# Performance work log

Hardware: AMD Instinct MI355X
Metric: run time of the kernel (lower is better)

## Reference

```python
import jax, jax.numpy as jnp
import numpy as np

SCALE = 0.08838834764831845  # 1/sqrt(head_dim=128)


def setup_inputs() -> dict:
    key = jax.random.key(0)
    kq, kk, kv = jax.random.split(key, 3)
    S, H, KVH, D = 2048, 32, 8, 128
    q = jax.random.normal(kq, (S, H, D), dtype=jnp.float32)
    k = jax.random.normal(kk, (S, KVH, D), dtype=jnp.float32)
    v = jax.random.normal(kv, (S, KVH, D), dtype=jnp.float32)
    return {"q": q, "k": k, "v": v}


def reference(q, k, v):
    # Prefill path without block tables -> _fallback_attention(q, k, v, scale, causal=True)
    S, H, D = q.shape
    kvh = k.shape[1]
    rep = H // kvh
    # GQA: repeat_interleave KV heads to match query heads
    k = jnp.repeat(k, rep, axis=1)  # [S, H, D]
    v = jnp.repeat(v, rep, axis=1)  # [S, H, D]
    # scores: [H, Sq, Sk]
    scores = jnp.einsum('qhd,khd->hqk', q, k) * SCALE
    # causal mask (seq_len_q == seq_len_k, diagonal=1 triu masked)
    causal = jnp.tril(jnp.ones((S, S), dtype=bool))
    scores = jnp.where(causal[None, :, :], scores, jnp.finfo(scores.dtype).min)
    attn = jax.nn.softmax(scores, axis=-1)
    out = jnp.einsum('hqk,khd->qhd', attn, v)  # [S, H, D]
    return out
```

## Files before the change

kernel.cpp:

```cpp
#include <hip/hip_runtime.h>


#define SEQ   2048
#define NH    32
#define NKVH  8
#define HD    128
#define BQ    128
#define BK    128
#define KSS   136
#define VTSF  72
#define PSS   72
#define SCALE 0.08838834764831845f
#define QS    (0.08838834764831845f * 1.4426950408889634f)

#define TILE_SH 16384
#define KB_ELEMS (SEQ * NKVH * HD)
#define WS_NEED  (2u * KB_ELEMS * 2u)

typedef __attribute__((ext_vector_type(8)))  short short8;
typedef __attribute__((ext_vector_type(16))) float float16;
typedef __attribute__((ext_vector_type(2)))  unsigned int uint2v;

__device__ __forceinline__ unsigned short f2bf(float f) {
    union { float f; unsigned int i; } x; x.f = f;
    unsigned int r = x.i + 0x7fffu + ((x.i >> 16) & 1u);
    return (unsigned short)(r >> 16);
}
__device__ __forceinline__ unsigned int f2bf2(float lo, float hi) {
    return (unsigned int)f2bf(lo) | ((unsigned int)f2bf(hi) << 16);
}
__device__ __forceinline__ unsigned int cvt_pk_bf16(float lo, float hi) {
    unsigned int r;
    asm("v_cvt_pk_bf16_f32 %0, %1, %2" : "=v"(r) : "v"(lo), "v"(hi));
    return r;
}

__device__ __forceinline__ void gload_lds16(const unsigned short* g, unsigned short* l) {
    __builtin_amdgcn_global_load_lds(
        (const __attribute__((address_space(1))) void*)g,
        (__attribute__((address_space(3))) void*)l, 16, 0, 0);
}

#if __has_builtin(__builtin_amdgcn_permlane32_swap)
#define PLSWAP(a, b, xout, yout) do { \
    uint2v r_ = __builtin_amdgcn_permlane32_swap((a), (b), false, false); \
    (xout) = r_.x; (yout) = r_.y; } while (0)
#else
#define PLSWAP(a, b, xout, yout) do { \
    unsigned int a_ = (a), b_ = (b); \
    asm volatile("s_nop 1\n\tv_permlane32_swap_b32 %0, %1" : "+v"(a_), "+v"(b_)); \
    (xout) = a_; (yout) = b_; } while (0)
#endif

#define MAKE_AF(dst, sv, b) do { \
    const unsigned int p0_ = cvt_pk_bf16(sv[(b) + 0], sv[(b) + 1]); \
    const unsigned int p1_ = cvt_pk_bf16(sv[(b) + 2], sv[(b) + 3]); \
    const unsigned int p2_ = cvt_pk_bf16(sv[(b) + 4], sv[(b) + 5]); \
    const unsigned int p3_ = cvt_pk_bf16(sv[(b) + 6], sv[(b) + 7]); \
    unsigned int w0_, w1_, w2_, w3_; \
    PLSWAP(p0_, p2_, w0_, w2_); \
    PLSWAP(p1_, p3_, w1_, w3_); \
    union { short8 v; unsigned int u[4]; } uu_; \
    uu_.u[0] = w0_; uu_.u[1] = w1_; uu_.u[2] = w2_; uu_.u[3] = w3_; \
    (dst) = uu_.v; } while (0)

__global__ __launch_bounds__(256)
void cvt_kv3(const float* __restrict__ k, const float* __restrict__ v,
             unsigned short* __restrict__ kws, unsigned short* __restrict__ vws)
{
    __shared__ unsigned short tl[128 * 144];
    const int t = threadIdx.x;
    if (blockIdx.x < 128) {
        const int bid = blockIdx.x;
        const int kvh = bid >> 4, tile = bid & 15;
        unsigned short* dst = kws + (size_t)bid * TILE_SH;
        #pragma unroll
        for (int r = 0; r < 8; ++r) {
            const int gid = r * 256 + t;
            const int gl = gid >> 7, row = gid & 127;
            const float* src =
                k + ((size_t)(tile * 128 + row) * NKVH + kvh) * HD + gl * 8;
            const float4 a = *(const float4*)(src);
            const float4 b = *(const float4*)(src + 4);
            uint4 o;
            o.x = f2bf2(a.x, a.y); o.y = f2bf2(a.z, a.w);
            o.z = f2bf2(b.x, b.y); o.w = f2bf2(b.z, b.w);
            *(uint4*)(dst + (size_t)gid * 8) = o;
        }
        return;
    }
    const int bid = blockIdx.x - 128;
    const int kvh = bid >> 4, tile = bid & 15;
    const int dp  = (t & 63) * 2;
    const int k0q = t >> 6;
    #pragma unroll
    for (int r = 0; r < 32; ++r) {
        const int key = k0q + r * 4;
        const float2 a =
            *(const float2*)(v + ((size_t)(tile * 128 + key) * NKVH + kvh) * HD + dp);
        tl[dp * 144 + key]       = f2bf(a.x);
        tl[(dp + 1) * 144 + key] = f2bf(a.y);
    }
    __syncthreads();
    unsigned short* dst = vws + (size_t)bid * TILE_SH;
    #pragma unroll
    for (int r = 0; r < 8; ++r) {
        const int gid = r * 256 + t;
        const int gl = gid >> 7, d = gid & 127;
        *(uint4*)(dst + (size_t)gid * 8) = *(const uint4*)&tl[d * 144 + gl * 8];
    }
}

__global__ __launch_bounds__(512, 1)
void attn_fwd8(const float* __restrict__ q,
               const unsigned short* __restrict__ kws,
               const unsigned short* __restrict__ vws,
               float* __restrict__ out)
{
    __shared__ __align__(16) unsigned char smem[131072];
    __shared__ float Sl[2][4][32];
    unsigned short* const ks0 = (unsigned short*)smem;
    unsigned short* const ks1 = (unsigned short*)(smem + 32768);
    unsigned short* const vt0 = (unsigned short*)(smem + 65536);
    unsigned short* const vt1 = (unsigned short*)(smem + 98304);
    float*          const obuf = (float*)smem;

    const int t    = threadIdx.x;
    const int w    = t >> 6;
    const int lane = t & 63;
    const int ln   = lane & 31;
    const int half = lane >> 5;
    const int g    = w >> 2;
    const int w3   = w & 3;

    const int bid = blockIdx.x;
    const int h   = (bid & 7) * 4 + ((bid >> 3) & 3);
    const int px  = bid >> 5;
    const int kvh = h >> 2;

    const int kofs = half * 1024 + (g * 64 + ln) * 8;
    const int vofs = (g * 8 + half) * 1024 + ln * 8;

    const unsigned short* const kgp = kws + (size_t)(kvh * 16) * TILE_SH + t * 8;
    const unsigned short* const vgp = vws + (size_t)(kvh * 16) * TILE_SH + t * 8;
    const int wofs = w * 512;

    short8 onesv;
    {
        union { short8 v; unsigned int u[4]; } uo;
        uo.u[0] = uo.u[1] = uo.u[2] = uo.u[3] = 0x3F803F80u;
        onesv = uo.v;
    }

#define ISSUE(tix, kb_, vb_) do { \
    const unsigned short* kg_ = kgp + (size_t)(tix) * TILE_SH; \
    const unsigned short* vg_ = vgp + (size_t)(tix) * TILE_SH; \
    gload_lds16(kg_,         (kb_) + wofs); \
    gload_lds16(kg_ +  4096, (kb_) + wofs + 4096); \
    gload_lds16(kg_ +  8192, (kb_) + wofs + 8192); \
    gload_lds16(kg_ + 12288, (kb_) + wofs + 12288); \
    gload_lds16(vg_,         (vb_) + wofs); \
    gload_lds16(vg_ +  4096, (vb_) + wofs + 4096); \
    gload_lds16(vg_ +  8192, (vb_) + wofs + 8192); \
    gload_lds16(vg_ + 12288, (vb_) + wofs + 12288); \
} while (0)

    for (int ph = 0; ph < 2; ++ph) {
        const int bx    = ph ? (15 - px) : px;
        const int q0    = bx * BQ;
        const int wq0   = q0 + w3 * 32;
        const int qrow  = wq0 + ln;
        const int wqmax = wq0 + 31;
        const int nit   = bx + 1;

        short8 qf[8];
        {
            const float* qr = q + ((size_t)qrow * NH + h) * HD;
            #pragma unroll
            for (int k0 = 0; k0 < 8; ++k0) {
                const float* p4 = qr + k0 * 16 + half * 8;
                const float4 a = *(const float4*)(p4);
                const float4 b = *(const float4*)(p4 + 4);
                union { short8 v; unsigned int u[4]; } uu;
                uu.u[0] = f2bf2(a.x * QS, a.y * QS);
                uu.u[1] = f2bf2(a.z * QS, a.w * QS);
                uu.u[2] = f2bf2(b.x * QS, b.y * QS);
                uu.u[3] = f2bf2(b.z * QS, b.w * QS);
                qf[k0] = uu.v;
            }
        }

        float16 o0, o1, o2, o3, lacc;
        #pragma unroll
        for (int i = 0; i < 16; ++i) {
            o0[i] = 0.f; o1[i] = 0.f; o2[i] = 0.f; o3[i] = 0.f; lacc[i] = 0.f;
        }

        ISSUE(0, ks0, vt0);
        if (nit > 1) ISSUE(1, ks1, vt1);

        for (int it = 0; it < nit; ++it) {
            const int cur = it & 1;
            const unsigned short* ksc = (cur ? ks1 : ks0) + kofs;
            const unsigned short* vtc = (cur ? vt1 : vt0) + vofs;

            if (it + 1 < nit) asm volatile("s_waitcnt vmcnt(8)" ::: "memory");
            else              asm volatile("s_waitcnt vmcnt(0)" ::: "memory");
            __builtin_amdgcn_s_barrier();
            __builtin_amdgcn_sched_barrier(0);

            const int j0g = it * BK + g * 64;
            if (j0g <= wqmax) {
                float16 st0, st1;
                #pragma unroll
                for (int i = 0; i < 16; ++i) { st0[i] = 0.f; st1[i] = 0.f; }
                __builtin_amdgcn_s_setprio(1);
                #pragma unroll
                for (int k0 = 0; k0 < 8; ++k0) {
                    const short8 a0 = *(const short8*)&ksc[k0 * 2048];
                    const short8 a1 = *(const short8*)&ksc[k0 * 2048 + 256];
                    st0 = __builtin_amdgcn_mfma_f32_32x32x16_bf16(a0, qf[k0], st0, 0, 0, 0);
                    st1 = __builtin_amdgcn_mfma_f32_32x32x16_bf16(a1, qf[k0], st1, 0, 0, 0);
                }
                __builtin_amdgcn_s_setprio(0);

                if ((j0g + 63) > wq0) {
                    #pragma unroll
                    for (int r = 0; r < 16; ++r) {
                        const int kl = (r & 3) + 8 * (r >> 2) + 4 * half;
                        if (j0g + kl > qrow)      st0[r] = -1e30f;
                        if (j0g + 32 + kl > qrow) st1[r] = -1e30f;
                    }
                }

#define PV_STEP(afx, kc) do { \
    const short8 bv0 = *(const short8*)&vtc[(kc) * 2048]; \
    const short8 bv1 = *(const short8*)&vtc[(kc) * 2048 + 256]; \
    const short8 bv2 = *(const short8*)&vtc[(kc) * 2048 + 512]; \
    const short8 bv3 = *(const short8*)&vtc[(kc) * 2048 + 768]; \
    o0 = __builtin_amdgcn_mfma_f32_32x32x16_bf16(afx, bv0, o0, 0, 0, 0); \
    o1 = __builtin_amdgcn_mfma_f32_32x32x16_bf16(afx, bv1, o1, 0, 0, 0); \
    o2 = __builtin_amdgcn_mfma_f32_32x32x16_bf16(afx, bv2, o2, 0, 0, 0); \
    o3 = __builtin_amdgcn_mfma_f32_32x32x16_bf16(afx, bv3, o3, 0, 0, 0); \
    lacc = __builtin_amdgcn_mfma_f32_32x32x16_bf16(afx, onesv, lacc, 0, 0, 0); \
} while (0)

                #pragma unroll
                for (int r = 0; r < 16; ++r) st0[r] = exp2f(st0[r]);
                short8 af0, af1;
                MAKE_AF(af0, st0, 0);
                MAKE_AF(af1, st0, 8);
                __builtin_amdgcn_s_setprio(1);
                PV_STEP(af0, 0);
                PV_STEP(af1, 1);
                __builtin_amdgcn_s_setprio(0);

                #pragma unroll
                for (int r = 0; r < 16; ++r) st1[r] = exp2f(st1[r]);
                short8 af2, af3;
                MAKE_AF(af2, st1, 0);
                MAKE_AF(af3, st1, 8);
                __builtin_amdgcn_s_setprio(1);
                PV_STEP(af2, 2);
                PV_STEP(af3, 3);
                __builtin_amdgcn_s_setprio(0);
#undef PV_STEP
            }

            asm volatile("s_waitcnt lgkmcnt(0)" ::: "memory");
            __builtin_amdgcn_s_barrier();
            __builtin_amdgcn_sched_barrier(0);
            if (it + 2 < nit) ISSUE(it + 2, cur ? ks1 : ks0, cur ? vt1 : vt0);
        }

        if (ln == 0) {
            #pragma unroll
            for (int r = 0; r < 16; ++r)
                Sl[g][w3][(r & 3) + 8 * (r >> 2) + 4 * half] = lacc[r];
        }
        __syncthreads();

        if (g == 1) {
            #pragma unroll
            for (int r = 0; r < 16; ++r) {
                const int rl = (r & 3) + 8 * (r >> 2) + 4 * half;
                float* ob = &obuf[(size_t)(w3 * 32 + rl) * 128];
                ob[ln]      = o0[r];
                ob[32 + ln] = o1[r];
                ob[64 + ln] = o2[r];
                ob[96 + ln] = o3[r];
            }
        }
        __syncthreads();
        if (g == 0) {
            #pragma unroll
            for (int r = 0; r < 16; ++r) {
                const int rl = (r & 3) + 8 * (r >> 2) + 4 * half;
                const float inv = 1.f / (Sl[0][w3][rl] + Sl[1][w3][rl]);
                const float* ob = &obuf[(size_t)(w3 * 32 + rl) * 128];
                float* orow = out + ((size_t)(wq0 + rl) * NH + h) * HD;
                orow[ln]      = (o0[r] + ob[ln])      * inv;
                orow[32 + ln] = (o1[r] + ob[32 + ln]) * inv;
                orow[64 + ln] = (o2[r] + ob[64 + ln]) * inv;
                orow[96 + ln] = (o3[r] + ob[96 + ln]) * inv;
            }
        }
        __syncthreads();
    }
#undef ISSUE
}

__global__ __launch_bounds__(256, 2)
void attn_fwd_fb(const float* __restrict__ q,
                 const float* __restrict__ k,
                 const float* __restrict__ v,
                 float* __restrict__ out)
{
    __shared__ unsigned short ks[64 * KSS];
    __shared__ unsigned short vt[HD * VTSF];
    __shared__ unsigned short ps[4][32 * PSS];
    __shared__ float          alf[4][32];

    const int t    = threadIdx.x;
    const int w    = t >> 6;
    const int lane = t & 63;
    const int ln   = lane & 31;
    const int half = lane >> 5;
    const int h    = blockIdx.y;
    const int kvh  = h >> 2;
    const int q0   = blockIdx.x * BQ;
    const int wq0  = q0 + w * 32;
    const int qrow = wq0 + ln;

    short8 qf[8];
    {
        const float* qr = q + ((size_t)qrow * NH + h) * HD;
        #pragma unroll
        for (int k0 = 0; k0 < 8; ++k0) {
            const float* p4 = qr + k0 * 16 + half * 8;
            const float4 a = *(const float4*)(p4);
            const float4 b = *(const float4*)(p4 + 4);
            union { short8 v; unsigned int u[4]; } uu;
            uu.u[0] = f2bf2(a.x, a.y);
            uu.u[1] = f2bf2(a.z, a.w);
            uu.u[2] = f2bf2(b.x, b.y);
            uu.u[3] = f2bf2(b.z, b.w);
            qf[k0] = uu.v;
        }
    }

    float16 o0, o1, o2, o3;
    #pragma unroll
    for (int i = 0; i < 16; ++i) { o0[i] = 0.f; o1[i] = 0.f; o2[i] = 0.f; o3[i] = 0.f; }
    float m_run = -1e30f, l_run = 0.f;
    const int ntiles = (q0 + BQ) / 64;
    const int wqmax  = wq0 + 31;

    for (int it = 0; it < ntiles; ++it) {
        const int j0 = it * 64;
        __syncthreads();
        {
            const int key = t >> 2;
            const int db  = (t & 3) * 4;
            const float* kr = k + ((size_t)(j0 + key) * NKVH + kvh) * HD;
            #pragma unroll
            for (int r2 = 0; r2 < 8; ++r2) {
                const int d = db + r2 * 16;
                const float4 a = *(const float4*)(kr + d);
                *(unsigned int*)&ks[key * KSS + d]     = f2bf2(a.x, a.y);
                *(unsigned int*)&ks[key * KSS + d + 2] = f2bf2(a.z, a.w);
            }
        }
        {
            const int kp = (t & 31) * 2;
            const int db = (t >> 5) * 4;
            const float* vr0 = v + ((size_t)(j0 + kp) * NKVH + kvh) * HD;
            const float* vr1 = vr0 + NKVH * HD;
            #pragma unroll
            for (int r2 = 0; r2 < 4; ++r2) {
                const int d = db + r2 * 32;
                const float4 a = *(const float4*)(vr0 + d);
                const float4 b = *(const float4*)(vr1 + d);
                *(unsigned int*)&vt[(d + 0) * VTSF + kp] = f2bf2(a.x, b.x);
                *(unsigned int*)&vt[(d + 1) * VTSF + kp] = f2bf2(a.y, b.y);
                *(unsigned int*)&vt[(d + 2) * VTSF + kp] = f2bf2(a.z, b.z);
                *(unsigned int*)&vt[(d + 3) * VTSF + kp] = f2bf2(a.w, b.w);
            }
        }
        __syncthreads();
        if (j0 > wqmax) continue;

        float16 st0, st1;
        #pragma unroll
        for (int i = 0; i < 16; ++i) { st0[i] = 0.f; st1[i] = 0.f; }
        #pragma unroll
        for (int k0 = 0; k0 < 8; ++k0) {
            const short8 a0 = *(const short8*)&ks[ln * KSS + k0 * 16 + half * 8];
            const short8 a1 = *(const short8*)&ks[(32 + ln) * KSS + k0 * 16 + half * 8];
            st0 = __builtin_amdgcn_mfma_f32_32x32x16_bf16(a0, qf[k0], st0, 0, 0, 0);
            st1 = __builtin_amdgcn_mfma_f32_32x32x16_bf16(a1, qf[k0], st1, 0, 0, 0);
        }
        const bool need_mask = (j0 + 63) > wq0;
        float mt = -1e30f;
        #pragma unroll
        for (int r = 0; r < 16; ++r) {
            const int kl = (r & 3) + 8 * (r >> 2) + 4 * half;
            float a0 = st0[r] * SCALE;
            float a1 = st1[r] * SCALE;
            if (need_mask) {
                if (j0 + kl > qrow)      a0 = -1e30f;
                if (j0 + 32 + kl > qrow) a1 = -1e30f;
            }
            st0[r] = a0; st1[r] = a1;
            mt = fmaxf(mt, fmaxf(a0, a1));
        }
        mt = fmaxf(mt, __shfl_xor(mt, 32, 64));
        const float mn = fmaxf(m_run, mt);
        float sm = 0.f;
        #pragma unroll
        for (int r = 0; r < 16; ++r) {
            const float e0 = __expf(st0[r] - mn);
            const float e1 = __expf(st1[r] - mn);
            st0[r] = e0; st1[r] = e1;
            sm += e0 + e1;
        }
        sm += __shfl_xor(sm, 32, 64);
        const float alpha = __expf(m_run - mn);
        m_run = mn;
        l_run = l_run * alpha + sm;

        unsigned short* psw = ps[w];
        #pragma unroll
        for (int r = 0; r < 16; r += 2) {
            const int kl = (r & 3) + 8 * (r >> 2) + 4 * half;
            *(unsigned int*)&psw[ln * PSS + kl]      = f2bf2(st0[r], st0[r + 1]);
            *(unsigned int*)&psw[ln * PSS + 32 + kl] = f2bf2(st1[r], st1[r + 1]);
        }
        if (half == 0) alf[w][ln] = alpha;
        #pragma unroll
        for (int r = 0; r < 16; ++r) {
            const int rl = (r & 3) + 8 * (r >> 2) + 4 * half;
            const float ar = alf[w][rl];
            o0[r] *= ar; o1[r] *= ar; o2[r] *= ar; o3[r] *= ar;
        }
        short8 af[4];
        #pragma unroll
        for (int kc = 0; kc < 4; ++kc)
            af[kc] = *(const short8*)&psw[ln * PSS + kc * 16 + half * 8];
        #pragma unroll
        for (int kc = 0; kc < 4; ++kc) {
            const short8 bv0 = *(const short8*)&vt[(ln)      * VTSF + kc * 16 + half * 8];
            const short8 bv1 = *(const short8*)&vt[(32 + ln) * VTSF + kc * 16 + half * 8];
            const short8 bv2 = *(const short8*)&vt[(64 + ln) * VTSF + kc * 16 + half * 8];
            const short8 bv3 = *(const short8*)&vt[(96 + ln) * VTSF + kc * 16 + half * 8];
            o0 = __builtin_amdgcn_mfma_f32_32x32x16_bf16(af[kc], bv0, o0, 0, 0, 0);
            o1 = __builtin_amdgcn_mfma_f32_32x32x16_bf16(af[kc], bv1, o1, 0, 0, 0);
            o2 = __builtin_amdgcn_mfma_f32_32x32x16_bf16(af[kc], bv2, o2, 0, 0, 0);
            o3 = __builtin_amdgcn_mfma_f32_32x32x16_bf16(af[kc], bv3, o3, 0, 0, 0);
        }
    }

    if (half == 0) alf[w][ln] = l_run;
    __builtin_amdgcn_s_waitcnt(0);
    #pragma unroll
    for (int r = 0; r < 16; ++r) {
        const int rl = (r & 3) + 8 * (r >> 2) + 4 * half;
        const float inv = 1.f / alf[w][rl];
        float* orow = out + ((size_t)(wq0 + rl) * NH + h) * HD;
        orow[ln]      = o0[r] * inv;
        orow[32 + ln] = o1[r] * inv;
        orow[64 + ln] = o2[r] * inv;
        orow[96 + ln] = o3[r] * inv;
    }
}

extern "C" void kernel_launch(void* const* d_in, const int* in_sizes, int n_in,
                              void* d_out, int out_size, void* d_ws, size_t ws_size,
                              hipStream_t stream) {
    const float* q = (const float*)d_in[0];
    const float* k = (const float*)d_in[1];
    const float* v = (const float*)d_in[2];
    float* out = (float*)d_out;
    if (ws_size >= (size_t)WS_NEED) {
        unsigned short* kws = (unsigned short*)d_ws;
        unsigned short* vws = kws + KB_ELEMS;
        cvt_kv3<<<256, 256, 0, stream>>>(k, v, kws, vws);
        attn_fwd8<<<256, 512, 0, stream>>>(q, kws, vws, out);
    } else {
        attn_fwd_fb<<<dim3(SEQ / BQ, NH), 256, 0, stream>>>(q, k, v, out);
    }
}
```

Before: 146.9 us.

## Software-pipeline PV matmul one iteration behind QK with triple-buffered V

Restructures the attention loop so the P·V MFMAs for the previous key tile run after the current tile's QK^T MFMAs. This overlaps exp/convert work with matrix-core work, and the P fragments are carried across iterations. V tiles move to a three-buffer rotation, raising LDS use to 160KB, and the softmax denominator scratch now reuses the LDS area. It also drops the explicit zeroing of the score accumulators by seeding the first MFMA with a zero vector. The cost is more live registers and a larger LDS footprint.

```diff
diff --git a/kernel.cpp b/kernel.cpp
--- a/kernel.cpp
+++ b/kernel.cpp
@@ -112,18 +112,19 @@
 }
 
 __global__ __launch_bounds__(512, 1)
-void attn_fwd8(const float* __restrict__ q,
+void attn_fwd9(const float* __restrict__ q,
                const unsigned short* __restrict__ kws,
                const unsigned short* __restrict__ vws,
                float* __restrict__ out)
 {
-    __shared__ __align__(16) unsigned char smem[131072];
-    __shared__ float Sl[2][4][32];
+    __shared__ __align__(16) unsigned char smem[163840];
     unsigned short* const ks0 = (unsigned short*)smem;
     unsigned short* const ks1 = (unsigned short*)(smem + 32768);
-    unsigned short* const vt0 = (unsigned short*)(smem + 65536);
-    unsigned short* const vt1 = (unsigned short*)(smem + 98304);
+    unsigned short* const vb0 = (unsigned short*)(smem + 65536);
+    unsigned short* const vb1 = (unsigned short*)(smem + 98304);
+    unsigned short* const vb2 = (unsigned short*)(smem + 131072);
     float*          const obuf = (float*)smem;
+    float*          const Slp  = (float*)(smem + 65536);
 
     const int t    = threadIdx.x;
     const int w    = t >> 6;
@@ -163,6 +164,23 @@
     gload_lds16(vg_ +  4096, (vb_) + wofs + 4096); \
     gload_lds16(vg_ +  8192, (vb_) + wofs + 8192); \
     gload_lds16(vg_ + 12288, (vb_) + wofs + 12288); \
+} while (0)
+
+#define PV4(base) do { \
+    const unsigned short* vp_ = (base) + vofs; \
+    _Pragma("unroll") \
+    for (int kc = 0; kc < 4; ++kc) { \
+        const short8 pa = (kc == 0) ? afp0 : (kc == 1) ? afp1 : (kc == 2) ? afp2 : afp3; \
+        const short8 bv0 = *(const short8*)&vp_[kc * 2048]; \
+        const short8 bv1 = *(const short8*)&vp_[kc * 2048 + 256]; \
+        const short8 bv2 = *(const short8*)&vp_[kc * 2048 + 512]; \
+        const short8 bv3 = *(const short8*)&vp_[kc * 2048 + 768]; \
+        o0 = __builtin_amdgcn_mfma_f32_32x32x16_bf16(pa, bv0, o0, 0, 0, 0); \
+        o1 = __builtin_amdgcn_mfma_f32_32x32x16_bf16(pa, bv1, o1, 0, 0, 0); \
+        o2 = __builtin_amdgcn_mfma_f32_32x32x16_bf16(pa, bv2, o2, 0, 0, 0); \
+        o3 = __builtin_amdgcn_mfma_f32_32x32x16_bf16(pa, bv3, o3, 0, 0, 0); \
+        lacc = __builtin_amdgcn_mfma_f32_32x32x16_bf16(pa, onesv, lacc, 0, 0, 0); \
+    } \
 } while (0)
 
     for (int ph = 0; ph < 2; ++ph) {
@@ -190,19 +208,26 @@
             }
         }
 
-        float16 o0, o1, o2, o3, lacc;
+        float16 o0, o1, o2, o3, lacc, z16;
         #pragma unroll
         for (int i = 0; i < 16; ++i) {
-            o0[i] = 0.f; o1[i] = 0.f; o2[i] = 0.f; o3[i] = 0.f; lacc[i] = 0.f;
-        }
-
-        ISSUE(0, ks0, vt0);
-        if (nit > 1) ISSUE(1, ks1, vt1);
+            o0[i] = 0.f; o1[i] = 0.f; o2[i] = 0.f; o3[i] = 0.f;
+            lacc[i] = 0.f; z16[i] = 0.f;
+        }
+
+        short8 afp0 = onesv, afp1 = onesv, afp2 = onesv, afp3 = onesv;
+        bool prevAct = false;
+
+        unsigned short* vA = vb0;
+        unsigned short* vB = vb1;
+        unsigned short* vC = vb2;
+
+        ISSUE(0, ks0, vb0);
+        if (nit > 1) ISSUE(1, ks1, vb1);
 
         for (int it = 0; it < nit; ++it) {
             const int cur = it & 1;
             const unsigned short* ksc = (cur ? ks1 : ks0) + kofs;
-            const unsigned short* vtc = (cur ? vt1 : vt0) + vofs;
 
             if (it + 1 < nit) asm volatile("s_waitcnt vmcnt(8)" ::: "memory");
             else              asm volatile("s_waitcnt vmcnt(0)" ::: "memory");
@@ -210,20 +235,34 @@
             __builtin_amdgcn_sched_barrier(0);
 
             const int j0g = it * BK + g * 64;
-            if (j0g <= wqmax) {
-                float16 st0, st1;
+            const bool curAct = (j0g <= wqmax);
+
+            float16 st0, st1;
+            if (curAct) {
+                __builtin_amdgcn_s_setprio(1);
+                {
+                    const short8 a0 = *(const short8*)&ksc[0];
+                    const short8 a1 = *(const short8*)&ksc[256];
+                    st0 = __builtin_amdgcn_mfma_f32_32x32x16_bf16(a0, qf[0], z16, 0, 0, 0);
+                    st1 = __builtin_amdgcn_mfma_f32_32x32x16_bf16(a1, qf[0], z16, 0, 0, 0);
+                }
                 #pragma unroll
-                for (int i = 0; i < 16; ++i) { st0[i] = 0.f; st1[i] = 0.f; }
-                __builtin_amdgcn_s_setprio(1);
-                #pragma unroll
-                for (int k0 = 0; k0 < 8; ++k0) {
+                for (int k0 = 1; k0 < 8; ++k0) {
                     const short8 a0 = *(const short8*)&ksc[k0 * 2048];
                     const short8 a1 = *(const short8*)&ksc[k0 * 2048 + 256];
                     st0 = __builtin_amdgcn_mfma_f32_32x32x16_bf16(a0, qf[k0], st0, 0, 0, 0);
                     st1 = __builtin_amdgcn_mfma_f32_32x32x16_bf16(a1, qf[k0], st1, 0, 0, 0);
                 }
                 __builtin_amdgcn_s_setprio(0);
-
+            }
+
+            if (prevAct) {
+                __builtin_amdgcn_s_setprio(1);
+                PV4(vC);
+                __builtin_amdgcn_s_setprio(0);
+            }
+
+            if (curAct) {
                 if ((j0g + 63) > wq0) {
                     #pragma unroll
                     for (int r = 0; r < 16; ++r) {
@@ -232,54 +271,33 @@
                         if (j0g + 32 + kl > qrow) st1[r] = -1e30f;
                     }
                 }
-
-#define PV_STEP(afx, kc) do { \
-    const short8 bv0 = *(const short8*)&vtc[(kc) * 2048]; \
-    const short8 bv1 = *(const short8*)&vtc[(kc) * 2048 + 256]; \
-    const short8 bv2 = *(const short8*)&vtc[(kc) * 2048 + 512]; \
-    const short8 bv3 = *(const short8*)&vtc[(kc) * 2048 + 768]; \
-    o0 = __builtin_amdgcn_mfma_f32_32x32x16_bf16(afx, bv0, o0, 0, 0, 0); \
-    o1 = __builtin_amdgcn_mfma_f32_32x32x16_bf16(afx, bv1, o1, 0, 0, 0); \
-    o2 = __builtin_amdgcn_mfma_f32_32x32x16_bf16(afx, bv2, o2, 0, 0, 0); \
-    o3 = __builtin_amdgcn_mfma_f32_32x32x16_bf16(afx, bv3, o3, 0, 0, 0); \
-    lacc = __builtin_amdgcn_mfma_f32_32x32x16_bf16(afx, onesv, lacc, 0, 0, 0); \
-} while (0)
-
                 #pragma unroll
                 for (int r = 0; r < 16; ++r) st0[r] = exp2f(st0[r]);
-                short8 af0, af1;
-                MAKE_AF(af0, st0, 0);
-                MAKE_AF(af1, st0, 8);
-                __builtin_amdgcn_s_setprio(1);
-                PV_STEP(af0, 0);
-                PV_STEP(af1, 1);
-                __builtin_amdgcn_s_setprio(0);
-
+                MAKE_AF(afp0, st0, 0);
+                MAKE_AF(afp1, st0, 8);
                 #pragma unroll
                 for (int r = 0; r < 16; ++r) st1[r] = exp2f(st1[r]);
-                short8 af2, af3;
-                MAKE_AF(af2, st1, 0);
-                MAKE_AF(af3, st1, 8);
-                __builtin_amdgcn_s_setprio(1);
-                PV_STEP(af2, 2);
-                PV_STEP(af3, 3);
-                __builtin_amdgcn_s_setprio(0);
-#undef PV_STEP
+                MAKE_AF(afp2, st1, 0);
+                MAKE_AF(afp3, st1, 8);
             }
 
             asm volatile("s_waitcnt lgkmcnt(0)" ::: "memory");
             __builtin_amdgcn_s_barrier();
             __builtin_amdgcn_sched_barrier(0);
-            if (it + 2 < nit) ISSUE(it + 2, cur ? ks1 : ks0, cur ? vt1 : vt0);
-        }
-
+            if (it + 2 < nit) ISSUE(it + 2, cur ? ks1 : ks0, vC);
+
+            unsigned short* tmp = vC; vC = vA; vA = vB; vB = tmp;
+            prevAct = curAct;
+        }
+
+        if (prevAct) PV4(vC);
+
+        __syncthreads();
         if (ln == 0) {
             #pragma unroll
             for (int r = 0; r < 16; ++r)
-                Sl[g][w3][(r & 3) + 8 * (r >> 2) + 4 * half] = lacc[r];
-        }
-        __syncthreads();
-
+                Slp[((g * 4 + w3) * 32) + ((r & 3) + 8 * (r >> 2) + 4 * half)] = lacc[r];
+        }
         if (g == 1) {
             #pragma unroll
             for (int r = 0; r < 16; ++r) {
@@ -296,7 +314,7 @@
             #pragma unroll
             for (int r = 0; r < 16; ++r) {
                 const int rl = (r & 3) + 8 * (r >> 2) + 4 * half;
-                const float inv = 1.f / (Sl[0][w3][rl] + Sl[1][w3][rl]);
+                const float inv = 1.f / (Slp[(w3 * 32) + rl] + Slp[((4 + w3) * 32) + rl]);
                 const float* ob = &obuf[(size_t)(w3 * 32 + rl) * 128];
                 float* orow = out + ((size_t)(wq0 + rl) * NH + h) * HD;
                 orow[ln]      = (o0[r] + ob[ln])      * inv;
@@ -307,6 +325,7 @@
         }
         __syncthreads();
     }
+#undef PV4
 #undef ISSUE
 }
 
@@ -485,7 +504,7 @@
         unsigned short* kws = (unsigned short*)d_ws;
         unsigned short* vws = kws + KB_ELEMS;
         cvt_kv3<<<256, 256, 0, stream>>>(k, v, kws, vws);
-        attn_fwd8<<<256, 512, 0, stream>>>(q, kws, vws, out);
+        attn_fwd9<<<256, 512, 0, stream>>>(q, kws, vws, out);
     } else {
         attn_fwd_fb<<<dim3(SEQ / BQ, NH), 256, 0, stream>>>(q, k, v, out);
     }
```

Result: slower. 151.1 us (+2.9%).

## Split KV loop across 512 smaller blocks with 64-key tiles and no cross-group reduction

Applied to the files above, without the earlier changes.

Replaces the 512-thread block, which split each 128-key tile across two wave groups and merged partial outputs through LDS, with 256-thread blocks that each own one query tile and step through 64-key tiles. The workspace layout is re-tiled to 64-key chunks, and the two causal phases become separate blocks (512 in total) at two blocks per CU. This drops the LDS reduction and its extra barriers and lets the scheduler balance light and heavy query tiles. In exchange it doubles the iteration count per tile, with more barriers per key processed and smaller prefetch chunks, and it removes the s_setprio hints.

```diff
diff --git a/kernel.cpp b/kernel.cpp
--- a/kernel.cpp
+++ b/kernel.cpp
@@ -6,14 +6,13 @@
 #define NKVH  8
 #define HD    128
 #define BQ    128
-#define BK    128
 #define KSS   136
 #define VTSF  72
 #define PSS   72
 #define SCALE 0.08838834764831845f
 #define QS    (0.08838834764831845f * 1.4426950408889634f)
 
-#define TILE_SH 16384
+#define T64_SH   8192
 #define KB_ELEMS (SEQ * NKVH * HD)
 #define WS_NEED  (2u * KB_ELEMS * 2u)
 
@@ -65,84 +64,91 @@
     (dst) = uu_.v; } while (0)
 
 __global__ __launch_bounds__(256)
-void cvt_kv3(const float* __restrict__ k, const float* __restrict__ v,
+void cvt_kv4(const float* __restrict__ k, const float* __restrict__ v,
              unsigned short* __restrict__ kws, unsigned short* __restrict__ vws)
 {
     __shared__ unsigned short tl[128 * 144];
     const int t = threadIdx.x;
     if (blockIdx.x < 128) {
-        const int bid = blockIdx.x;
-        const int kvh = bid >> 4, tile = bid & 15;
-        unsigned short* dst = kws + (size_t)bid * TILE_SH;
-        #pragma unroll
-        for (int r = 0; r < 8; ++r) {
-            const int gid = r * 256 + t;
+        const int bid  = blockIdx.x;
+        const int kvh  = bid >> 4, t128 = bid & 15;
+        unsigned short* dst = kws + ((size_t)(kvh * 32) + t128 * 2) * T64_SH;
+        #pragma unroll
+        for (int rr = 0; rr < 8; ++rr) {
+            const int gid = rr * 256 + t;
             const int gl = gid >> 7, row = gid & 127;
             const float* src =
-                k + ((size_t)(tile * 128 + row) * NKVH + kvh) * HD + gl * 8;
+                k + ((size_t)(t128 * 128 + row) * NKVH + kvh) * HD + gl * 8;
             const float4 a = *(const float4*)(src);
             const float4 b = *(const float4*)(src + 4);
             uint4 o;
             o.x = f2bf2(a.x, a.y); o.y = f2bf2(a.z, a.w);
             o.z = f2bf2(b.x, b.y); o.w = f2bf2(b.z, b.w);
-            *(uint4*)(dst + (size_t)gid * 8) = o;
+            const size_t off = (size_t)(row >> 6) * T64_SH + (gl * 64 + (row & 63)) * 8;
+            *(uint4*)(dst + off) = o;
         }
         return;
     }
-    const int bid = blockIdx.x - 128;
-    const int kvh = bid >> 4, tile = bid & 15;
-    const int dp  = (t & 63) * 2;
-    const int k0q = t >> 6;
-    #pragma unroll
-    for (int r = 0; r < 32; ++r) {
-        const int key = k0q + r * 4;
+    const int bid  = blockIdx.x - 128;
+    const int kvh  = bid >> 4, t128 = bid & 15;
+    const int dp   = (t & 63) * 2;
+    const int k0q  = t >> 6;
+    #pragma unroll
+    for (int rr = 0; rr < 32; ++rr) {
+        const int key = k0q + rr * 4;
         const float2 a =
-            *(const float2*)(v + ((size_t)(tile * 128 + key) * NKVH + kvh) * HD + dp);
+            *(const float2*)(v + ((size_t)(t128 * 128 + key) * NKVH + kvh) * HD + dp);
         tl[dp * 144 + key]       = f2bf(a.x);
         tl[(dp + 1) * 144 + key] = f2bf(a.y);
     }
     __syncthreads();
-    unsigned short* dst = vws + (size_t)bid * TILE_SH;
-    #pragma unroll
-    for (int r = 0; r < 8; ++r) {
-        const int gid = r * 256 + t;
-        const int gl = gid >> 7, d = gid & 127;
-        *(uint4*)(dst + (size_t)gid * 8) = *(const uint4*)&tl[d * 144 + gl * 8];
-    }
-}
-
-__global__ __launch_bounds__(512, 1)
-void attn_fwd8(const float* __restrict__ q,
-               const unsigned short* __restrict__ kws,
-               const unsigned short* __restrict__ vws,
-               float* __restrict__ out)
+    unsigned short* dst = vws + ((size_t)(kvh * 32) + t128 * 2) * T64_SH;
+    #pragma unroll
+    for (int rr = 0; rr < 8; ++rr) {
+        const int gid = rr * 256 + t;
+        const int d = gid & 127, gk = gid >> 7;
+        const size_t off = (size_t)(gk >> 3) * T64_SH + (((gk & 7) * 128) + d) * 8;
+        *(uint4*)(dst + off) = *(const uint4*)&tl[d * 144 + gk * 8];
+    }
+}
+
+__global__ __launch_bounds__(256, 2)
+void attn_fwd11(const float* __restrict__ q,
+                const unsigned short* __restrict__ kws,
+                const unsigned short* __restrict__ vws,
+                float* __restrict__ out)
 {
-    __shared__ __align__(16) unsigned char smem[131072];
-    __shared__ float Sl[2][4][32];
-    unsigned short* const ks0 = (unsigned short*)smem;
-    unsigned short* const ks1 = (unsigned short*)(smem + 32768);
-    unsigned short* const vt0 = (unsigned short*)(smem + 65536);
-    unsigned short* const vt1 = (unsigned short*)(smem + 98304);
-    float*          const obuf = (float*)smem;
+    __shared__ __align__(16) unsigned short smem[32768];
+    unsigned short* const ks0 = smem;
+    unsigned short* const ks1 = smem + 8192;
+    unsigned short* const vt0 = smem + 16384;
+    unsigned short* const vt1 = smem + 24576;
 
     const int t    = threadIdx.x;
     const int w    = t >> 6;
     const int lane = t & 63;
     const int ln   = lane & 31;
     const int half = lane >> 5;
-    const int g    = w >> 2;
-    const int w3   = w & 3;
-
-    const int bid = blockIdx.x;
-    const int h   = (bid & 7) * 4 + ((bid >> 3) & 3);
-    const int px  = bid >> 5;
-    const int kvh = h >> 2;
-
-    const int kofs = half * 1024 + (g * 64 + ln) * 8;
-    const int vofs = (g * 8 + half) * 1024 + ln * 8;
-
-    const unsigned short* const kgp = kws + (size_t)(kvh * 16) * TILE_SH + t * 8;
-    const unsigned short* const vgp = vws + (size_t)(kvh * 16) * TILE_SH + t * 8;
+
+    const int bid  = blockIdx.x;
+    const int pair = bid & 255;
+    const int late = bid >> 8;
+    const int h    = (pair & 7) * 4 + ((pair >> 3) & 3);
+    const int px   = pair >> 5;
+    const int bx   = late ? (15 - px) : px;
+    const int kvh  = h >> 2;
+
+    const int q0    = bx * BQ;
+    const int wq0   = q0 + w * 32;
+    const int qrow  = wq0 + ln;
+    const int wqmax = wq0 + 31;
+    const int nit   = 2 * bx + 2;
+
+    const int kofs = half * 512 + ln * 8;
+    const int vofs = half * 1024 + ln * 8;
+
+    const unsigned short* const kgp = kws + (size_t)(kvh * 32) * T64_SH + t * 8;
+    const unsigned short* const vgp = vws + (size_t)(kvh * 32) * T64_SH + t * 8;
     const int wofs = w * 512;
 
     short8 onesv;
@@ -153,85 +159,80 @@
     }
 
 #define ISSUE(tix, kb_, vb_) do { \
-    const unsigned short* kg_ = kgp + (size_t)(tix) * TILE_SH; \
-    const unsigned short* vg_ = vgp + (size_t)(tix) * TILE_SH; \
-    gload_lds16(kg_,         (kb_) + wofs); \
-    gload_lds16(kg_ +  4096, (kb_) + wofs + 4096); \
-    gload_lds16(kg_ +  8192, (kb_) + wofs + 8192); \
-    gload_lds16(kg_ + 12288, (kb_) + wofs + 12288); \
-    gload_lds16(vg_,         (vb_) + wofs); \
-    gload_lds16(vg_ +  4096, (vb_) + wofs + 4096); \
-    gload_lds16(vg_ +  8192, (vb_) + wofs + 8192); \
-    gload_lds16(vg_ + 12288, (vb_) + wofs + 12288); \
+    const unsigned short* kg_ = kgp + (size_t)(tix) * T64_SH; \
+    const unsigned short* vg_ = vgp + (size_t)(tix) * T64_SH; \
+    gload_lds16(kg_,        (kb_) + wofs); \
+    gload_lds16(kg_ + 2048, (kb_) + wofs + 2048); \
+    gload_lds16(kg_ + 4096, (kb_) + wofs + 4096); \
+    gload_lds16(kg_ + 6144, (kb_) + wofs + 6144); \
+    gload_lds16(vg_,        (vb_) + wofs); \
+    gload_lds16(vg_ + 2048, (vb_) + wofs + 2048); \
+    gload_lds16(vg_ + 4096, (vb_) + wofs + 4096); \
+    gload_lds16(vg_ + 6144, (vb_) + wofs + 6144); \
 } while (0)
 
-    for (int ph = 0; ph < 2; ++ph) {
-        const int bx    = ph ? (15 - px) : px;
-        const int q0    = bx * BQ;
-        const int wq0   = q0 + w3 * 32;
-        const int qrow  = wq0 + ln;
-        const int wqmax = wq0 + 31;
-        const int nit   = bx + 1;
-
-        short8 qf[8];
-        {
-            const float* qr = q + ((size_t)qrow * NH + h) * HD;
+    short8 qf[8];
+    {
+        const float* qr = q + ((size_t)qrow * NH + h) * HD;
+        #pragma unroll
+        for (int k0 = 0; k0 < 8; ++k0) {
+            const float* p4 = qr + k0 * 16 + half * 8;
+            const float4 a = *(const float4*)(p4);
+            const float4 b = *(const float4*)(p4 + 4);
+            union { short8 v; unsigned int u[4]; } uu;
+            uu.u[0] = f2bf2(a.x * QS, a.y * QS);
+            uu.u[1] = f2bf2(a.z * QS, a.w * QS);
+            uu.u[2] = f2bf2(b.x * QS, b.y * QS);
+            uu.u[3] = f2bf2(b.z * QS, b.w * QS);
+            qf[k0] = uu.v;
+        }
+    }
+
+    float16 o0, o1, o2, o3, lacc, z16;
+    #pragma unroll
+    for (int i = 0; i < 16; ++i) {
+        o0[i] = 0.f; o1[i] = 0.f; o2[i] = 0.f; o3[i] = 0.f;
+        lacc[i] = 0.f; z16[i] = 0.f;
+    }
+
+    ISSUE(0, ks0, vt0);
+    ISSUE(1, ks1, vt1);
+
+    for (int it = 0; it < nit; ++it) {
+        const int cur = it & 1;
+        const unsigned short* ksc = (cur ? ks1 : ks0) + kofs;
+        const unsigned short* vtc = (cur ? vt1 : vt0) + vofs;
+
+        if (it + 1 < nit) asm volatile("s_waitcnt vmcnt(8)" ::: "memory");
+        else              asm volatile("s_waitcnt vmcnt(0)" ::: "memory");
+        __builtin_amdgcn_s_barrier();
+        __builtin_amdgcn_sched_barrier(0);
+
+        const int j0 = it * 64;
+        if (j0 <= wqmax) {
+            float16 st0, st1;
+            {
+                const short8 a0 = *(const short8*)&ksc[0];
+                const short8 a1 = *(const short8*)&ksc[256];
+                st0 = __builtin_amdgcn_mfma_f32_32x32x16_bf16(a0, qf[0], z16, 0, 0, 0);
+                st1 = __builtin_amdgcn_mfma_f32_32x32x16_bf16(a1, qf[0], z16, 0, 0, 0);
+            }
             #pragma unroll
-            for (int k0 = 0; k0 < 8; ++k0) {
-                const float* p4 = qr + k0 * 16 + half * 8;
-                const float4 a = *(const float4*)(p4);
-                const float4 b = *(const float4*)(p4 + 4);
-                union { short8 v; unsigned int u[4]; } uu;
-                uu.u[0] = f2bf2(a.x * QS, a.y * QS);
-                uu.u[1] = f2bf2(a.z * QS, a.w * QS);
-                uu.u[2] = f2bf2(b.x * QS, b.y * QS);
-                uu.u[3] = f2bf2(b.z * QS, b.w * QS);
-                qf[k0] = uu.v;
-            }
-        }
-
-        float16 o0, o1, o2, o3, lacc;
-        #pragma unroll
-        for (int i = 0; i < 16; ++i) {
-            o0[i] = 0.f; o1[i] = 0.f; o2[i] = 0.f; o3[i] = 0.f; lacc[i] = 0.f;
-        }
-
-        ISSUE(0, ks0, vt0);
-        if (nit > 1) ISSUE(1, ks1, vt1);
-
-        for (int it = 0; it < nit; ++it) {
-            const int cur = it & 1;
-            const unsigned short* ksc = (cur ? ks1 : ks0) + kofs;
-            const unsigned short* vtc = (cur ? vt1 : vt0) + vofs;
-
-            if (it + 1 < nit) asm volatile("s_waitcnt vmcnt(8)" ::: "memory");
-            else              asm volatile("s_waitcnt vmcnt(0)" ::: "memory");
-            __builtin_amdgcn_s_barrier();
-            __builtin_amdgcn_sched_barrier(0);
-
-            const int j0g = it * BK + g * 64;
-            if (j0g <= wqmax) {
-                float16 st0, st1;
+            for (int k0 = 1; k0 < 8; ++k0) {
+                const short8 a0 = *(const short8*)&ksc[k0 * 1024];
+                const short8 a1 = *(const short8*)&ksc[k0 * 1024 + 256];
+                st0 = __builtin_amdgcn_mfma_f32_32x32x16_bf16(a0, qf[k0], st0, 0, 0, 0);
+                st1 = __builtin_amdgcn_mfma_f32_32x32x16_bf16(a1, qf[k0], st1, 0, 0, 0);
+            }
+
+            if ((j0 + 63) > wq0) {
                 #pragma unroll
-                for (int i = 0; i < 16; ++i) { st0[i] = 0.f; st1[i] = 0.f; }
-                __builtin_amdgcn_s_setprio(1);
-                #pragma unroll
-                for (int k0 = 0; k0 < 8; ++k0) {
-                    const short8 a0 = *(const short8*)&ksc[k0 * 2048];
-                    const short8 a1 = *(const short8*)&ksc[k0 * 2048 + 256];
-                    st0 = __builtin_amdgcn_mfma_f32_32x32x16_bf16(a0, qf[k0], st0, 0, 0, 0);
-                    st1 = __builtin_amdgcn_mfma_f32_32x32x16_bf16(a1, qf[k0], st1, 0, 0, 0);
+                for (int r = 0; r < 16; ++r) {
+                    const int kl = (r & 3) + 8 * (r >> 2) + 4 * half;
+                    if (j0 + kl > qrow)      st0[r] = -1e30f;
+                    if (j0 + 32 + kl > qrow) st1[r] = -1e30f;
                 }
-                __builtin_amdgcn_s_setprio(0);
-
-                if ((j0g + 63) > wq0) {
-                    #pragma unroll
-                    for (int r = 0; r < 16; ++r) {
-                        const int kl = (r & 3) + 8 * (r >> 2) + 4 * half;
-                        if (j0g + kl > qrow)      st0[r] = -1e30f;
-                        if (j0g + 32 + kl > qrow) st1[r] = -1e30f;
-                    }
-                }
+            }
 
 #define PV_STEP(afx, kc) do { \
     const short8 bv0 = *(const short8*)&vtc[(kc) * 2048]; \
@@ -245,67 +246,39 @@
     lacc = __builtin_amdgcn_mfma_f32_32x32x16_bf16(afx, onesv, lacc, 0, 0, 0); \
 } while (0)
 
-                #pragma unroll
-                for (int r = 0; r < 16; ++r) st0[r] = exp2f(st0[r]);
-                short8 af0, af1;
-                MAKE_AF(af0, st0, 0);
-                MAKE_AF(af1, st0, 8);
-                __builtin_amdgcn_s_setprio(1);
-                PV_STEP(af0, 0);
-                PV_STEP(af1, 1);
-                __builtin_amdgcn_s_setprio(0);
-
-                #pragma unroll
-                for (int r = 0; r < 16; ++r) st1[r] = exp2f(st1[r]);
-                short8 af2, af3;
-                MAKE_AF(af2, st1, 0);
-                MAKE_AF(af3, st1, 8);
-                __builtin_amdgcn_s_setprio(1);
-                PV_STEP(af2, 2);
-                PV_STEP(af3, 3);
-                __builtin_amdgcn_s_setprio(0);
+            #pragma unroll
+            for (int r = 0; r < 16; ++r) st0[r] = exp2f(st0[r]);
+            short8 af0, af1;
+            MAKE_AF(af0, st0, 0);
+            MAKE_AF(af1, st0, 8);
+            PV_STEP(af0, 0);
+            PV_STEP(af1, 1);
+
+            #pragma unroll
+            for (int r = 0; r < 16; ++r) st1[r] = exp2f(st1[r]);
+            short8 af2, af3;
+            MAKE_AF(af2, st1, 0);
+            MAKE_AF(af3, st1, 8);
+            PV_STEP(af2, 2);
+            PV_STEP(af3, 3);
 #undef PV_STEP
-            }
-
-            asm volatile("s_waitcnt lgkmcnt(0)" ::: "memory");
-            __builtin_amdgcn_s_barrier();
-            __builtin_amdgcn_sched_barrier(0);
-            if (it + 2 < nit) ISSUE(it + 2, cur ? ks1 : ks0, cur ? vt1 : vt0);
-        }
-
-        if (ln == 0) {
-            #pragma unroll
-            for (int r = 0; r < 16; ++r)
-                Sl[g][w3][(r & 3) + 8 * (r >> 2) + 4 * half] = lacc[r];
-        }
-        __syncthreads();
-
-        if (g == 1) {
-            #pragma unroll
-            for (int r = 0; r < 16; ++r) {
-                const int rl = (r & 3) + 8 * (r >> 2) + 4 * half;
-                float* ob = &obuf[(size_t)(w3 * 32 + rl) * 128];
-                ob[ln]      = o0[r];
-                ob[32 + ln] = o1[r];
-                ob[64 + ln] = o2[r];
-                ob[96 + ln] = o3[r];
-            }
-        }
-        __syncthreads();
-        if (g == 0) {
-            #pragma unroll
-            for (int r = 0; r < 16; ++r) {
-                const int rl = (r & 3) + 8 * (r >> 2) + 4 * half;
-                const float inv = 1.f / (Sl[0][w3][rl] + Sl[1][w3][rl]);
-                const float* ob = &obuf[(size_t)(w3 * 32 + rl) * 128];
-                float* orow = out + ((size_t)(wq0 + rl) * NH + h) * HD;
-                orow[ln]      = (o0[r] + ob[ln])      * inv;
-                orow[32 + ln] = (o1[r] + ob[32 + ln]) * inv;
-                orow[64 + ln] = (o2[r] + ob[64 + ln]) * inv;
-                orow[96 + ln] = (o3[r] + ob[96 + ln]) * inv;
-            }
-        }
-        __syncthreads();
+        }
+
+        asm volatile("s_waitcnt lgkmcnt(0)" ::: "memory");
+        __builtin_amdgcn_s_barrier();
+        __builtin_amdgcn_sched_barrier(0);
+        if (it + 2 < nit) ISSUE(it + 2, cur ? ks1 : ks0, cur ? vt1 : vt0);
+    }
+
+    #pragma unroll
+    for (int r = 0; r < 16; ++r) {
+        const int rl = (r & 3) + 8 * (r >> 2) + 4 * half;
+        const float inv = 1.f / lacc[r];
+        float* orow = out + ((size_t)(wq0 + rl) * NH + h) * HD;
+        orow[ln]      = o0[r] * inv;
+        orow[32 + ln] = o1[r] * inv;
+        orow[64 + ln] = o2[r] * inv;
+        orow[96 + ln] = o3[r] * inv;
     }
 #undef ISSUE
 }
@@ -484,8 +457,8 @@
     if (ws_size >= (size_t)WS_NEED) {
         unsigned short* kws = (unsigned short*)d_ws;
         unsigned short* vws = kws + KB_ELEMS;
-        cvt_kv3<<<256, 256, 0, stream>>>(k, v, kws, vws);
-        attn_fwd8<<<256, 512, 0, stream>>>(q, kws, vws, out);
+        cvt_kv4<<<256, 256, 0, stream>>>(k, v, kws, vws);
+        attn_fwd11<<<512, 256, 0, stream>>>(q, kws, vws, out);
     } else {
         attn_fwd_fb<<<dim3(SEQ / BQ, NH), 256, 0, stream>>>(q, k, v, out);
     }
```

New measurement: 151.5 us. +3.1%, slower.

## Load V fragments directly from global memory instead of staging through LDS

Applied to the files above, without the earlier changes.

The V tile is no longer copied into shared memory. Each wave reads its V B-operand fragments straight from the pre-converted global workspace into registers, issuing the loads early so they overlap the QK MFMAs. Shared memory drops to 64KB, holding only the double-buffered K. K fragments are also hoisted into registers before the QK MFMA chain, and the setprio hints are removed. This cuts LDS traffic and async copy count, but exposes global/L2 latency inside the compute loop and raises register pressure.

```diff
diff --git a/kernel.cpp b/kernel.cpp
--- a/kernel.cpp
+++ b/kernel.cpp
@@ -112,17 +112,15 @@
 }
 
 __global__ __launch_bounds__(512, 1)
-void attn_fwd8(const float* __restrict__ q,
-               const unsigned short* __restrict__ kws,
-               const unsigned short* __restrict__ vws,
-               float* __restrict__ out)
+void attn_fwd12(const float* __restrict__ q,
+                const unsigned short* __restrict__ kws,
+                const unsigned short* __restrict__ vws,
+                float* __restrict__ out)
 {
-    __shared__ __align__(16) unsigned char smem[131072];
+    __shared__ __align__(16) unsigned char smem[65536];
     __shared__ float Sl[2][4][32];
     unsigned short* const ks0 = (unsigned short*)smem;
     unsigned short* const ks1 = (unsigned short*)(smem + 32768);
-    unsigned short* const vt0 = (unsigned short*)(smem + 65536);
-    unsigned short* const vt1 = (unsigned short*)(smem + 98304);
     float*          const obuf = (float*)smem;
 
     const int t    = threadIdx.x;
@@ -142,7 +140,7 @@
     const int vofs = (g * 8 + half) * 1024 + ln * 8;
 
     const unsigned short* const kgp = kws + (size_t)(kvh * 16) * TILE_SH + t * 8;
-    const unsigned short* const vgp = vws + (size_t)(kvh * 16) * TILE_SH + t * 8;
+    const unsigned short* const vt0 = vws + (size_t)(kvh * 16) * TILE_SH + vofs;
     const int wofs = w * 512;
 
     short8 onesv;
@@ -152,17 +150,20 @@
         onesv = uo.v;
     }
 
-#define ISSUE(tix, kb_, vb_) do { \
+#define ISSUE(tix, kb_) do { \
     const unsigned short* kg_ = kgp + (size_t)(tix) * TILE_SH; \
-    const unsigned short* vg_ = vgp + (size_t)(tix) * TILE_SH; \
     gload_lds16(kg_,         (kb_) + wofs); \
     gload_lds16(kg_ +  4096, (kb_) + wofs + 4096); \
     gload_lds16(kg_ +  8192, (kb_) + wofs + 8192); \
     gload_lds16(kg_ + 12288, (kb_) + wofs + 12288); \
-    gload_lds16(vg_,         (vb_) + wofs); \
-    gload_lds16(vg_ +  4096, (vb_) + wofs + 4096); \
-    gload_lds16(vg_ +  8192, (vb_) + wofs + 8192); \
-    gload_lds16(vg_ + 12288, (vb_) + wofs + 12288); \
+} while (0)
+
+#define PV_R(afx, b0, b1, b2, b3) do { \
+    o0 = __builtin_amdgcn_mfma_f32_32x32x16_bf16(afx, b0, o0, 0, 0, 0); \
+    o1 = __builtin_amdgcn_mfma_f32_32x32x16_bf16(afx, b1, o1, 0, 0, 0); \
+    o2 = __builtin_amdgcn_mfma_f32_32x32x16_bf16(afx, b2, o2, 0, 0, 0); \
+    o3 = __builtin_amdgcn_mfma_f32_32x32x16_bf16(afx, b3, o3, 0, 0, 0); \
+    lacc = __builtin_amdgcn_mfma_f32_32x32x16_bf16(afx, onesv, lacc, 0, 0, 0); \
 } while (0)
 
     for (int ph = 0; ph < 2; ++ph) {
@@ -190,39 +191,60 @@
             }
         }
 
-        float16 o0, o1, o2, o3, lacc;
+        float16 o0, o1, o2, o3, lacc, z16;
         #pragma unroll
         for (int i = 0; i < 16; ++i) {
-            o0[i] = 0.f; o1[i] = 0.f; o2[i] = 0.f; o3[i] = 0.f; lacc[i] = 0.f;
-        }
-
-        ISSUE(0, ks0, vt0);
-        if (nit > 1) ISSUE(1, ks1, vt1);
+            o0[i] = 0.f; o1[i] = 0.f; o2[i] = 0.f; o3[i] = 0.f;
+            lacc[i] = 0.f; z16[i] = 0.f;
+        }
+
+        ISSUE(0, ks0);
+        if (nit > 1) ISSUE(1, ks1);
 
         for (int it = 0; it < nit; ++it) {
             const int cur = it & 1;
             const unsigned short* ksc = (cur ? ks1 : ks0) + kofs;
-            const unsigned short* vtc = (cur ? vt1 : vt0) + vofs;
-
-            if (it + 1 < nit) asm volatile("s_waitcnt vmcnt(8)" ::: "memory");
+            const unsigned short* vg  = vt0 + (size_t)it * TILE_SH;
+
+            if (it + 1 < nit) asm volatile("s_waitcnt vmcnt(4)" ::: "memory");
             else              asm volatile("s_waitcnt vmcnt(0)" ::: "memory");
             __builtin_amdgcn_s_barrier();
             __builtin_amdgcn_sched_barrier(0);
 
             const int j0g = it * BK + g * 64;
             if (j0g <= wqmax) {
-                float16 st0, st1;
-                #pragma unroll
-                for (int i = 0; i < 16; ++i) { st0[i] = 0.f; st1[i] = 0.f; }
-                __builtin_amdgcn_s_setprio(1);
+                const short8 vv00 = *(const short8*)&vg[0];
+                const short8 vv01 = *(const short8*)&vg[256];
+                const short8 vv02 = *(const short8*)&vg[512];
+                const short8 vv03 = *(const short8*)&vg[768];
+
+                short8 ka[16];
                 #pragma unroll
                 for (int k0 = 0; k0 < 8; ++k0) {
-                    const short8 a0 = *(const short8*)&ksc[k0 * 2048];
-                    const short8 a1 = *(const short8*)&ksc[k0 * 2048 + 256];
-                    st0 = __builtin_amdgcn_mfma_f32_32x32x16_bf16(a0, qf[k0], st0, 0, 0, 0);
-                    st1 = __builtin_amdgcn_mfma_f32_32x32x16_bf16(a1, qf[k0], st1, 0, 0, 0);
+                    ka[2 * k0]     = *(const short8*)&ksc[k0 * 2048];
+                    ka[2 * k0 + 1] = *(const short8*)&ksc[k0 * 2048 + 256];
                 }
-                __builtin_amdgcn_s_setprio(0);
+                float16 st0, st1;
+                st0 = __builtin_amdgcn_mfma_f32_32x32x16_bf16(ka[0], qf[0], z16, 0, 0, 0);
+                st1 = __builtin_amdgcn_mfma_f32_32x32x16_bf16(ka[1], qf[0], z16, 0, 0, 0);
+                #pragma unroll
+                for (int k0 = 1; k0 < 8; ++k0) {
+                    st0 = __builtin_amdgcn_mfma_f32_32x32x16_bf16(ka[2 * k0],     qf[k0], st0, 0, 0, 0);
+                    st1 = __builtin_amdgcn_mfma_f32_32x32x16_bf16(ka[2 * k0 + 1], qf[k0], st1, 0, 0, 0);
+                }
+
+                const short8 vv10 = *(const short8*)&vg[2048];
+                const short8 vv11 = *(const short8*)&vg[2048 + 256];
+                const short8 vv12 = *(const short8*)&vg[2048 + 512];
+                const short8 vv13 = *(const short8*)&vg[2048 + 768];
+                const short8 vv20 = *(const short8*)&vg[4096];
+                const short8 vv21 = *(const short8*)&vg[4096 + 256];
+                const short8 vv22 = *(const short8*)&vg[4096 + 512];
+                const short8 vv23 = *(const short8*)&vg[4096 + 768];
+                const short8 vv30 = *(const short8*)&vg[6144];
+                const short8 vv31 = *(const short8*)&vg[6144 + 256];
+                const short8 vv32 = *(const short8*)&vg[6144 + 512];
+                const short8 vv33 = *(const short8*)&vg[6144 + 768];
 
                 if ((j0g + 63) > wq0) {
                     #pragma unroll
@@ -233,44 +255,27 @@
                     }
                 }
 
-#define PV_STEP(afx, kc) do { \
-    const short8 bv0 = *(const short8*)&vtc[(kc) * 2048]; \
-    const short8 bv1 = *(const short8*)&vtc[(kc) * 2048 + 256]; \
-    const short8 bv2 = *(const short8*)&vtc[(kc) * 2048 + 512]; \
-    const short8 bv3 = *(const short8*)&vtc[(kc) * 2048 + 768]; \
-    o0 = __builtin_amdgcn_mfma_f32_32x32x16_bf16(afx, bv0, o0, 0, 0, 0); \
-    o1 = __builtin_amdgcn_mfma_f32_32x32x16_bf16(afx, bv1, o1, 0, 0, 0); \
-    o2 = __builtin_amdgcn_mfma_f32_32x32x16_bf16(afx, bv2, o2, 0, 0, 0); \
-    o3 = __builtin_amdgcn_mfma_f32_32x32x16_bf16(afx, bv3, o3, 0, 0, 0); \
-    lacc = __builtin_amdgcn_mfma_f32_32x32x16_bf16(afx, onesv, lacc, 0, 0, 0); \
-} while (0)
-
                 #pragma unroll
                 for (int r = 0; r < 16; ++r) st0[r] = exp2f(st0[r]);
                 short8 af0, af1;
                 MAKE_AF(af0, st0, 0);
                 MAKE_AF(af1, st0, 8);
-                __builtin_amdgcn_s_setprio(1);
-                PV_STEP(af0, 0);
-                PV_STEP(af1, 1);
-                __builtin_amdgcn_s_setprio(0);
+                PV_R(af0, vv00, vv01, vv02, vv03);
+                PV_R(af1, vv10, vv11, vv12, vv13);
 
                 #pragma unroll
                 for (int r = 0; r < 16; ++r) st1[r] = exp2f(st1[r]);
                 short8 af2, af3;
                 MAKE_AF(af2, st1, 0);
                 MAKE_AF(af3, st1, 8);
-                __builtin_amdgcn_s_setprio(1);
-                PV_STEP(af2, 2);
-                PV_STEP(af3, 3);
-                __builtin_amdgcn_s_setprio(0);
-#undef PV_STEP
+                PV_R(af2, vv20, vv21, vv22, vv23);
+                PV_R(af3, vv30, vv31, vv32, vv33);
             }
 
             asm volatile("s_waitcnt lgkmcnt(0)" ::: "memory");
             __builtin_amdgcn_s_barrier();
             __builtin_amdgcn_sched_barrier(0);
-            if (it + 2 < nit) ISSUE(it + 2, cur ? ks1 : ks0, cur ? vt1 : vt0);
+            if (it + 2 < nit) ISSUE(it + 2, cur ? ks1 : ks0);
         }
 
         if (ln == 0) {
@@ -307,6 +312,7 @@
         }
         __syncthreads();
     }
+#undef PV_R
 #undef ISSUE
 }
 
@@ -485,7 +491,7 @@
         unsigned short* kws = (unsigned short*)d_ws;
         unsigned short* vws = kws + KB_ELEMS;
         cvt_kv3<<<256, 256, 0, stream>>>(k, v, kws, vws);
-        attn_fwd8<<<256, 512, 0, stream>>>(q, kws, vws, out);
+        attn_fwd12<<<256, 512, 0, stream>>>(q, kws, vws, out);
     } else {
         attn_fwd_fb<<<dim3(SEQ / BQ, NH), 256, 0, stream>>>(q, k, v, out);
     }
```

Result: slower. 149.9 us (+2.1%).
